# Performance work log

Hardware: AMD Instinct MI355X
Metric: run time of the kernel (lower is better)

The kernel has to match this reference:

```python
import jax, jax.numpy as jnp
import numpy as np

N_NODES = 50000
N_EDGES = 800000
N_FEAT = 128
HIDDEN = 64
N_GRAPHS = 256


def setup_inputs() -> dict:
    key = jax.random.key(0)
    ks = jax.random.split(key, 10)
    x = jax.random.normal(ks[0], (N_NODES, N_FEAT), dtype=jnp.float32)
    edge_index = jax.random.randint(ks[1], (2, N_EDGES), 0, N_NODES, dtype=jnp.int64)
    batch = jnp.sort(jax.random.randint(ks[2], (N_NODES,), 0, N_GRAPHS, dtype=jnp.int64))
    s1 = 1.0 / np.sqrt(N_FEAT)
    s2 = 1.0 / np.sqrt(HIDDEN)
    W1 = jax.random.normal(ks[3], (N_FEAT, HIDDEN), dtype=jnp.float32) * s1
    b1 = jnp.zeros((HIDDEN,), dtype=jnp.float32)
    W2 = jax.random.normal(ks[4], (HIDDEN, HIDDEN), dtype=jnp.float32) * s2
    b2 = jnp.zeros((HIDDEN,), dtype=jnp.float32)
    Wm1 = jax.random.normal(ks[5], (HIDDEN, HIDDEN), dtype=jnp.float32) * s2
    bm1 = jnp.zeros((HIDDEN,), dtype=jnp.float32)
    Wm2 = jax.random.normal(ks[6], (HIDDEN, 1), dtype=jnp.float32) * s2
    bm2 = jnp.zeros((1,), dtype=jnp.float32)
    return {"x": x, "edge_index": edge_index, "batch": batch,
            "W1": W1, "b1": b1, "W2": W2, "b2": b2,
            "Wm1": Wm1, "bm1": bm1, "Wm2": Wm2, "bm2": bm2}


def _gcn_layer(h, W, b, src, dst, norm, n_nodes):
    # GCNConv: h @ W, then symmetric-normalized scatter-add over edges (+ self-loops), + bias
    h = h @ W
    msg = h[src] * norm[:, None]              # [E+N, H] gather + scale
    agg = jax.ops.segment_sum(msg, dst, num_segments=n_nodes)
    return agg + b


def reference(x, edge_index, batch, W1, b1, W2, b2, Wm1, bm1, Wm2, bm2):
    n = x.shape[0]
    loops = jnp.arange(n, dtype=edge_index.dtype)
    src = jnp.concatenate([edge_index[0], loops])  # self-loops as in PyG GCNConv
    dst = jnp.concatenate([edge_index[1], loops])
    deg = jax.ops.segment_sum(jnp.ones_like(dst, dtype=x.dtype), dst, num_segments=n)
    dis = jnp.where(deg > 0, jax.lax.rsqrt(deg), 0.0)  # deg^-1/2
    norm = dis[src] * dis[dst]

    h = jax.nn.relu(_gcn_layer(x, W1, b1, src, dst, norm, n))
    h = jax.nn.relu(_gcn_layer(h, W2, b2, src, dst, norm, n))

    # global mean pool over graphs
    sums = jax.ops.segment_sum(h, batch, num_segments=N_GRAPHS)
    cnts = jax.ops.segment_sum(jnp.ones((n,), dtype=h.dtype), batch, num_segments=N_GRAPHS)
    pooled = sums / jnp.maximum(cnts, 1.0)[:, None]

    # MLP head (dropout inactive at eval)
    out = jax.nn.relu(pooled @ Wm1 + bm1) @ Wm2 + bm2
    return out.reshape(-1)
```

## Files before the change

### kernel.cpp

```cpp
#include <hip/hip_runtime.h>

#define NN 50000
#define NE 800000
#define NF 128
#define NH 64
#define NG 256
#define NB 196
#define NC 196
#define CH 4096
#define CELL 80
#define CAP 5120
#define NGB 782

typedef __attribute__((ext_vector_type(8))) short bf16x8;
typedef __attribute__((ext_vector_type(4))) float f32x4;

static __device__ __forceinline__ unsigned short f2bf(float f) {
    union { float f; unsigned u; } v; v.f = f;
    unsigned r = v.u + 0x7FFF + ((v.u >> 16) & 1);
    return (unsigned short)(r >> 16);
}
static __device__ __forceinline__ float lo16(unsigned u) {
    return __uint_as_float(u << 16);
}
static __device__ __forceinline__ float hi16(unsigned u) {
    return __uint_as_float(u & 0xFFFF0000u);
}
static __device__ __forceinline__ unsigned pack2(float a, float b) {
    return (unsigned)f2bf(a) | ((unsigned)f2bf(b) << 16);
}

__global__ __launch_bounds__(256) void prep_gemm(const int* __restrict__ ei,
                                                 int* __restrict__ histg,
                                                 unsigned* __restrict__ ebuf,
                                                 const float* __restrict__ X,
                                                 const float* __restrict__ W,
                                                 const float* __restrict__ W2,
                                                 unsigned short* __restrict__ Y,
                                                 float* __restrict__ psum,
                                                 unsigned* __restrict__ W2p) {
    __shared__ __align__(16) char smem[35840];
    const int t = threadIdx.x;

    if (blockIdx.x < NC) {
        int* hist = (int*)smem;
        int* incl = hist + 256;
        int* lcur = incl + 256;
        int* wq   = lcur + 256;
        unsigned* lpairs = (unsigned*)(smem + 4096);
        const int c = blockIdx.x;
        const int c0 = c * CH;

        hist[t] = 0;
        __syncthreads();

        int es[16], ed[16];
#pragma unroll
        for (int j = 0; j < 4; ++j) {
            const int e = c0 + (j * 256 + t) * 4;
            int4 s4 = make_int4(-1, -1, -1, -1);
            int4 d4 = make_int4(-1, -1, -1, -1);
            if (e + 3 < NE) {
                s4 = *(const int4*)&ei[e];
                d4 = *(const int4*)&ei[NE + e];
            } else {
                if (e < NE)     { s4.x = ei[e];     d4.x = ei[NE + e]; }
                if (e + 1 < NE) { s4.y = ei[e + 1]; d4.y = ei[NE + e + 1]; }
                if (e + 2 < NE) { s4.z = ei[e + 2]; d4.z = ei[NE + e + 2]; }
            }
            es[4*j] = s4.x; es[4*j+1] = s4.y; es[4*j+2] = s4.z; es[4*j+3] = s4.w;
            ed[4*j] = d4.x; ed[4*j+1] = d4.y; ed[4*j+2] = d4.z; ed[4*j+3] = d4.w;
            if (d4.x >= 0) atomicAdd(&hist[d4.x >> 8], 1);
            if (d4.y >= 0) atomicAdd(&hist[d4.y >> 8], 1);
            if (d4.z >= 0) atomicAdd(&hist[d4.z >> 8], 1);
            if (d4.w >= 0) atomicAdd(&hist[d4.w >> 8], 1);
        }
        __syncthreads();

        const int v = hist[t];
        int sv = v;
#pragma unroll
        for (int off = 1; off < 64; off <<= 1) {
            int u = __shfl_up(sv, off, 64);
            if ((t & 63) >= off) sv += u;
        }
        if ((t & 63) == 63) wq[t >> 6] = sv;
        __syncthreads();
        {
            const int wid = t >> 6;
            int add = 0;
            if (wid > 0) add += wq[0];
            if (wid > 1) add += wq[1];
            if (wid > 2) add += wq[2];
            sv += add;
        }
        incl[t] = sv;
        lcur[t] = sv - v;
        if (t < NB) histg[c * NB + t] = v;
        __syncthreads();

#pragma unroll
        for (int j = 0; j < 16; ++j) {
            const int d = ed[j];
            if (d >= 0) {
                int p = atomicAdd(&lcur[d >> 8], 1);
                lpairs[p] = (unsigned)es[j] | ((unsigned)d << 16);
            }
        }
        __syncthreads();

        const int total = incl[255];
        for (int p = t; p < total; p += 256) {
            const unsigned pr = lpairs[p];
            const int b = pr >> 24;
            const int i = p - (incl[b] - hist[b]);
            ebuf[(b * NC + c) * CELL + i] = pr;
        }
    } else {
        const int gb = blockIdx.x - NC;
        if (gb >= NGB) {
            for (int idx = t; idx < 2048; idx += 256) {
                const int n = idx >> 5, kp = idx & 31;
                W2p[idx] = pack2(W2[(2 * kp) * 64 + n], W2[(2 * kp + 1) * 64 + n]);
            }
            return;
        }
        if (gb < 17) {
            const int o = gb * 1024 + t * 4;
            if (o < 16640) *(float4*)&psum[o] = make_float4(0.f, 0.f, 0.f, 0.f);
        }

        unsigned short* Xs = (unsigned short*)smem;
        unsigned int* Wt = (unsigned int*)(smem + 17408);
        const int base = gb * 64;

        for (int i = t * 4; i < 64 * 128; i += 1024) {
            int node = i >> 7, k = i & 127;
            int gn = base + node; if (gn >= NN) gn = NN - 1;
            float4 v = *(const float4*)&X[(size_t)gn * 128 + k];
            ushort4 o = { f2bf(v.x), f2bf(v.y), f2bf(v.z), f2bf(v.w) };
            *(ushort4*)&Xs[node * 136 + k] = o;
        }
        for (int idx = t; idx < 64 * 64; idx += 256) {
            int n = idx & 63, kp = idx >> 6;
            float w0 = W[(2 * kp) * 64 + n];
            float w1 = W[(2 * kp + 1) * 64 + n];
            Wt[n * 68 + kp] = (unsigned)f2bf(w0) | ((unsigned)f2bf(w1) << 16);
        }
        __syncthreads();

        const int w = t >> 6;
        const int lane = t & 63;
        const int l15 = lane & 15;
        const int quad = lane >> 4;
        f32x4 acc[4] = {{0.f,0.f,0.f,0.f},{0.f,0.f,0.f,0.f},{0.f,0.f,0.f,0.f},{0.f,0.f,0.f,0.f}};
#pragma unroll
        for (int kk = 0; kk < 4; ++kk) {
            const bf16x8 a = *(const bf16x8*)&Xs[(w * 16 + l15) * 136 + quad * 8 + kk * 32];
#pragma unroll
            for (int nt = 0; nt < 4; ++nt) {
                const bf16x8 b = *(const bf16x8*)&Wt[(nt * 16 + l15) * 68 + quad * 4 + kk * 16];
                acc[nt] = __builtin_amdgcn_mfma_f32_16x16x32_bf16(a, b, acc[nt], 0, 0, 0);
            }
        }
        const int r0 = base + w * 16 + quad * 4;
#pragma unroll
        for (int reg = 0; reg < 4; ++reg) {
            const int row = r0 + reg;
            if (row < NN) {
#pragma unroll
                for (int nt = 0; nt < 4; ++nt)
                    Y[(size_t)row * 64 + nt * 16 + l15] = f2bf(acc[nt][reg]);
            }
        }
    }
}

__global__ __launch_bounds__(512) void build_csr(const unsigned* __restrict__ ebuf,
                                                 const int* __restrict__ histg,
                                                 int2* __restrict__ row_range,
                                                 float* __restrict__ dis,
                                                 int* __restrict__ csr_src) {
    const int b = blockIdx.x, t = threadIdx.x;
    const int e0 = b * CAP;
    __shared__ int coffs[256];
    __shared__ int cvs[256];
    __shared__ int deg_l[256];
    __shared__ int pre[256];
    __shared__ int cur[256];
    __shared__ int wq[8];
    __shared__ unsigned lpairs[CAP];
    __shared__ int lsrc[CAP];

    int cv = 0;
    if (t < NC) cv = histg[t * NB + b];
    int sv = cv;
    if (t < 256) {
#pragma unroll
        for (int off = 1; off < 64; off <<= 1) {
            int u = __shfl_up(sv, off, 64);
            if ((t & 63) >= off) sv += u;
        }
        if ((t & 63) == 63) wq[t >> 6] = sv;
        deg_l[t] = (b * 256 + t < NN) ? 1 : 0;
        cvs[t] = cv;
    }
    __syncthreads();
    if (t < 256) {
        const int wid = t >> 6;
        int add = 0;
        if (wid > 0) add += wq[0];
        if (wid > 1) add += wq[1];
        if (wid > 2) add += wq[2];
        coffs[t] = sv + add;
    }
    __syncthreads();

    {
        const int tc = t & 255;
        const int cv2 = cvs[tc];
        if (tc < NC && cv2 > 0) {
            const uint4* src4 = (const uint4*)&ebuf[(size_t)(b * NC + tc) * CELL];
            const int dst = coffs[tc] - cv2;
            for (int g4 = (t >> 8); g4 * 4 < cv2; g4 += 2) {
                const uint4 u = src4[g4];
                const int i = g4 * 4;
                lpairs[dst + i] = u.x;
                if (i + 1 < cv2) lpairs[dst + i + 1] = u.y;
                if (i + 2 < cv2) lpairs[dst + i + 2] = u.z;
                if (i + 3 < cv2) lpairs[dst + i + 3] = u.w;
            }
        }
    }
    __syncthreads();

    const int total = coffs[255];
    for (int i = t; i < total; i += 512)
        atomicAdd(&deg_l[(lpairs[i] >> 16) & 255], 1);
    __syncthreads();

    int dvi = 0, psv = 0;
    if (t < 256) {
        dvi = deg_l[t];
        psv = dvi;
#pragma unroll
        for (int off = 1; off < 64; off <<= 1) {
            int u = __shfl_up(psv, off, 64);
            if ((t & 63) >= off) psv += u;
        }
        if ((t & 63) == 63) wq[4 + (t >> 6)] = psv;
    }
    __syncthreads();
    if (t < 256) {
        const int wid = t >> 6;
        int add = 0;
        if (wid > 0) add += wq[4];
        if (wid > 1) add += wq[5];
        if (wid > 2) add += wq[6];
        psv += add;
        pre[t] = psv;
        cur[t] = 1;
        const int nd = b * 256 + t;
        if (nd < NN) {
            const int excl = psv - dvi;
            lsrc[excl] = nd;
            row_range[nd] = make_int2(e0 + excl, e0 + psv);
            dis[nd] = rsqrtf((float)dvi);
        }
    }
    __syncthreads();

    for (int i = t; i < total; i += 512) {
        const unsigned p = lpairs[i];
        const int d = (p >> 16) & 255;
        const int pos = (pre[d] - deg_l[d]) + atomicAdd(&cur[d], 1);
        lsrc[pos] = (int)(p & 0xFFFFu);
    }
    __syncthreads();
    const int tot_all = pre[255];
    for (int i = t; i < tot_all; i += 512)
        csr_src[e0 + i] = lsrc[i];
}

static __device__ __forceinline__ void acc8(float* acc, const uint4 u) {
    acc[0] += lo16(u.x); acc[1] += hi16(u.x);
    acc[2] += lo16(u.y); acc[3] += hi16(u.y);
    acc[4] += lo16(u.z); acc[5] += hi16(u.z);
    acc[6] += lo16(u.w); acc[7] += hi16(u.w);
}
static __device__ __forceinline__ void fma8(float* acc, const uint4 u, const float d) {
    acc[0] = fmaf(lo16(u.x), d, acc[0]); acc[1] = fmaf(hi16(u.x), d, acc[1]);
    acc[2] = fmaf(lo16(u.y), d, acc[2]); acc[3] = fmaf(hi16(u.y), d, acc[3]);
    acc[4] = fmaf(lo16(u.z), d, acc[4]); acc[5] = fmaf(hi16(u.z), d, acc[5]);
    acc[6] = fmaf(lo16(u.w), d, acc[6]); acc[7] = fmaf(hi16(u.w), d, acc[7]);
}

static __device__ __forceinline__ void gather_rows(const unsigned short* __restrict__ h,
                                                   const int* __restrict__ csr,
                                                   int lo, int hi, int p8, float* acc) {
    int i = lo;
    for (; i + 8 <= hi; i += 8) {
        int idx[8];
#pragma unroll
        for (int j = 0; j < 8; ++j) idx[j] = csr[i + j];
        uint4 u[8];
#pragma unroll
        for (int j = 0; j < 8; ++j) u[j] = *(const uint4*)&h[(idx[j] << 6) + p8];
#pragma unroll
        for (int j = 0; j < 8; ++j) acc8(acc, u[j]);
    }
    if (i + 4 <= hi) {
        int idx[4];
#pragma unroll
        for (int j = 0; j < 4; ++j) idx[j] = csr[i + j];
        uint4 u[4];
#pragma unroll
        for (int j = 0; j < 4; ++j) u[j] = *(const uint4*)&h[(idx[j] << 6) + p8];
#pragma unroll
        for (int j = 0; j < 4; ++j) acc8(acc, u[j]);
        i += 4;
    }
    if (i + 2 <= hi) {
        const int i0 = csr[i], i1 = csr[i + 1];
        const uint4 u0 = *(const uint4*)&h[(i0 << 6) + p8];
        const uint4 u1 = *(const uint4*)&h[(i1 << 6) + p8];
        acc8(acc, u0); acc8(acc, u1);
        i += 2;
    }
    if (i < hi) acc8(acc, *(const uint4*)&h[(csr[i] << 6) + p8]);
}

static __device__ __forceinline__ void gather_rows_scaled(const unsigned short* __restrict__ h,
                                                          const int* __restrict__ csr,
                                                          const float* __restrict__ dis,
                                                          int lo, int hi, int p8, float* acc) {
    int i = lo;
    for (; i + 8 <= hi; i += 8) {
        int idx[8];
#pragma unroll
        for (int j = 0; j < 8; ++j) idx[j] = csr[i + j];
        float d[8];
#pragma unroll
        for (int j = 0; j < 8; ++j) d[j] = dis[idx[j]];
        uint4 u[8];
#pragma unroll
        for (int j = 0; j < 8; ++j) u[j] = *(const uint4*)&h[(idx[j] << 6) + p8];
#pragma unroll
        for (int j = 0; j < 8; ++j) fma8(acc, u[j], d[j]);
    }
    if (i + 4 <= hi) {
        int idx[4];
#pragma unroll
        for (int j = 0; j < 4; ++j) idx[j] = csr[i + j];
        float d[4];
#pragma unroll
        for (int j = 0; j < 4; ++j) d[j] = dis[idx[j]];
        uint4 u[4];
#pragma unroll
        for (int j = 0; j < 4; ++j) u[j] = *(const uint4*)&h[(idx[j] << 6) + p8];
#pragma unroll
        for (int j = 0; j < 4; ++j) fma8(acc, u[j], d[j]);
        i += 4;
    }
    if (i + 2 <= hi) {
        const int i0 = csr[i], i1 = csr[i + 1];
        const float d0 = dis[i0], d1 = dis[i1];
        const uint4 u0 = *(const uint4*)&h[(i0 << 6) + p8];
        const uint4 u1 = *(const uint4*)&h[(i1 << 6) + p8];
        fma8(acc, u0, d0); fma8(acc, u1, d1);
        i += 2;
    }
    if (i < hi) {
        const int i0 = csr[i];
        fma8(acc, *(const uint4*)&h[(i0 << 6) + p8], dis[i0]);
    }
}

__global__ __launch_bounds__(256) void agg_gemv(const unsigned short* __restrict__ h,
                                                const int2* __restrict__ row_range,
                                                const int* __restrict__ csr_src,
                                                const float* __restrict__ dis,
                                                const float* __restrict__ b1,
                                                const unsigned* __restrict__ W2p,
                                                unsigned short* __restrict__ g) {
    __shared__ unsigned short W2b[64 * 72];
    __shared__ unsigned short A[32 * 72];
    const int t = threadIdx.x;
    const int base = blockIdx.x * 32;
    const int nloc = t >> 3;
    const int p8 = (t & 7) * 8;
    const int n = base + nloc;
    float acc[8] = {};
    if (n < NN) {
        const int2 rr = row_range[n];
        gather_rows_scaled(h, csr_src, dis, rr.x, rr.y, p8, acc);
        const float dn = dis[n];
        const float4 bv0 = *(const float4*)&b1[p8];
        const float4 bv1 = *(const float4*)&b1[p8 + 4];
        acc[0] = fmaxf(acc[0] * dn + bv0.x, 0.f);
        acc[1] = fmaxf(acc[1] * dn + bv0.y, 0.f);
        acc[2] = fmaxf(acc[2] * dn + bv0.z, 0.f);
        acc[3] = fmaxf(acc[3] * dn + bv0.w, 0.f);
        acc[4] = fmaxf(acc[4] * dn + bv1.x, 0.f);
        acc[5] = fmaxf(acc[5] * dn + bv1.y, 0.f);
        acc[6] = fmaxf(acc[6] * dn + bv1.z, 0.f);
        acc[7] = fmaxf(acc[7] * dn + bv1.w, 0.f);
    }
    for (int idx = t; idx < 2048; idx += 256) {
        const int nn2 = idx >> 5, kp = idx & 31;
        *(unsigned*)&W2b[nn2 * 72 + 2 * kp] = W2p[idx];
    }
    uint4 pk;
    pk.x = pack2(acc[0], acc[1]);
    pk.y = pack2(acc[2], acc[3]);
    pk.z = pack2(acc[4], acc[5]);
    pk.w = pack2(acc[6], acc[7]);
    *(uint4*)&A[nloc * 72 + p8] = pk;
    __syncthreads();

    const int w = t >> 6;
    const int lane = t & 63;
    const int l15 = lane & 15;
    const int quad = lane >> 4;
    const int mt = w & 1;
    const int nq = (w >> 1) * 2;
    const bf16x8 a0 = *(const bf16x8*)&A[(mt * 16 + l15) * 72 + quad * 8];
    const bf16x8 a1 = *(const bf16x8*)&A[(mt * 16 + l15) * 72 + 32 + quad * 8];
    const bf16x8 b00 = *(const bf16x8*)&W2b[(nq * 16 + l15) * 72 + quad * 8];
    const bf16x8 b01 = *(const bf16x8*)&W2b[(nq * 16 + l15) * 72 + 32 + quad * 8];
    const bf16x8 b10 = *(const bf16x8*)&W2b[((nq + 1) * 16 + l15) * 72 + quad * 8];
    const bf16x8 b11 = *(const bf16x8*)&W2b[((nq + 1) * 16 + l15) * 72 + 32 + quad * 8];
    f32x4 c0 = {0.f, 0.f, 0.f, 0.f}, c1 = {0.f, 0.f, 0.f, 0.f};
    c0 = __builtin_amdgcn_mfma_f32_16x16x32_bf16(a0, b00, c0, 0, 0, 0);
    c0 = __builtin_amdgcn_mfma_f32_16x16x32_bf16(a1, b01, c0, 0, 0, 0);
    c1 = __builtin_amdgcn_mfma_f32_16x16x32_bf16(a0, b10, c1, 0, 0, 0);
    c1 = __builtin_amdgcn_mfma_f32_16x16x32_bf16(a1, b11, c1, 0, 0, 0);
    const int r0 = base + mt * 16 + quad * 4;
    float4 d4 = *(const float4*)&dis[r0];
    const float dd[4] = { d4.x, d4.y, d4.z, d4.w };
#pragma unroll
    for (int reg = 0; reg < 4; ++reg) {
        const int row = r0 + reg;
        if (row < NN) {
            g[(size_t)row * 64 + nq * 16 + l15] = f2bf(c0[reg] * dd[reg]);
            g[(size_t)row * 64 + (nq + 1) * 16 + l15] = f2bf(c1[reg] * dd[reg]);
        }
    }
}

__global__ __launch_bounds__(256) void agg_pool(const unsigned short* __restrict__ h,
                                                const int2* __restrict__ row_range,
                                                const int* __restrict__ csr_src,
                                                const float* __restrict__ dis,
                                                const float* __restrict__ bias,
                                                const int* __restrict__ batch,
                                                float* __restrict__ psum,
                                                float* __restrict__ cnt) {
    __shared__ float rowsL[32 * 68];
    __shared__ int nb[32];
    const int t = threadIdx.x;
    const int nloc = t >> 3;
    const int n = blockIdx.x * 32 + nloc;
    const int p8 = (t & 7) * 8;
    if ((t & 7) == 0) nb[nloc] = (n < NN) ? batch[n] : -1;
    if (n < NN) {
        const int2 rr = row_range[n];
        float acc[8] = {};
        gather_rows(h, csr_src, rr.x, rr.y, p8, acc);
        const float dn = dis[n];
        const float4 bv0 = *(const float4*)&bias[p8];
        const float4 bv1 = *(const float4*)&bias[p8 + 4];
        float4 r0, r1;
        r0.x = fmaxf(acc[0] * dn + bv0.x, 0.f);
        r0.y = fmaxf(acc[1] * dn + bv0.y, 0.f);
        r0.z = fmaxf(acc[2] * dn + bv0.z, 0.f);
        r0.w = fmaxf(acc[3] * dn + bv0.w, 0.f);
        r1.x = fmaxf(acc[4] * dn + bv1.x, 0.f);
        r1.y = fmaxf(acc[5] * dn + bv1.y, 0.f);
        r1.z = fmaxf(acc[6] * dn + bv1.z, 0.f);
        r1.w = fmaxf(acc[7] * dn + bv1.w, 0.f);
        *(float4*)&rowsL[nloc * 68 + p8] = r0;
        *(float4*)&rowsL[nloc * 68 + p8 + 4] = r1;
    }
    __syncthreads();
    if (t < 64) {
        float s = 0.f; int curg = -2; int rl = 0;
        for (int r = 0; r < 32; ++r) {
            const int gg = nb[r];
            if (gg != curg) {
                if (curg >= 0) {
                    atomicAdd(&psum[curg * 64 + t], s);
                    if (t == 0) atomicAdd(&cnt[curg], (float)rl);
                }
                s = 0.f; rl = 0; curg = gg;
            }
            if (gg >= 0) { s += rowsL[r * 68 + t]; ++rl; }
        }
        if (curg >= 0) {
            atomicAdd(&psum[curg * 64 + t], s);
            if (t == 0) atomicAdd(&cnt[curg], (float)rl);
        }
    }
}

__global__ __launch_bounds__(64) void head_kernel(const float* __restrict__ psum,
                                                  const float* __restrict__ cnt,
                                                  const float* __restrict__ Wm1,
                                                  const float* __restrict__ bm1,
                                                  const float* __restrict__ Wm2,
                                                  const float* __restrict__ bm2,
                                                  float* __restrict__ out) {
    const int g = blockIdx.x;
    const int t = threadIdx.x;
    __shared__ float pl[64];
    const float inv = 1.f / fmaxf(cnt[g], 1.f);
    pl[t] = psum[g * 64 + t] * inv;
    __syncthreads();
    float z = bm1[t];
#pragma unroll 8
    for (int k = 0; k < 64; ++k)
        z += pl[k] * Wm1[k * 64 + t];
    z = fmaxf(z, 0.f);
    float y = z * Wm2[t];
    for (int off = 32; off; off >>= 1) y += __shfl_down(y, off);
    if (t == 0) out[g] = y + bm2[0];
}

extern "C" void kernel_launch(void* const* d_in, const int* in_sizes, int n_in,
                              void* d_out, int out_size, void* d_ws, size_t ws_size,
                              hipStream_t stream) {
    const float* x   = (const float*)d_in[0];
    const int*   ei  = (const int*)d_in[1];
    const int*   bat = (const int*)d_in[2];
    const float* W1  = (const float*)d_in[3];
    const float* b1  = (const float*)d_in[4];
    const float* W2  = (const float*)d_in[5];
    const float* b2  = (const float*)d_in[6];
    const float* Wm1 = (const float*)d_in[7];
    const float* bm1 = (const float*)d_in[8];
    const float* Wm2 = (const float*)d_in[9];
    const float* bm2 = (const float*)d_in[10];
    float* out = (float*)d_out;

    char* w = (char*)d_ws;
    int*            histg     = (int*)           (w + 0);
    int2*           row_range = (int2*)          (w + 153664);
    float*          dis       = (float*)         (w + 553664);
    int*            csr_src   = (int*)           (w + 753664);
    unsigned*       ebuf      = (unsigned*)      (w + 4767744);
    unsigned short* bufA      = (unsigned short*)(w + 17060864);
    unsigned short* bufB      = (unsigned short*)(w + 23460864);
    float*          psum      = (float*)         (w + 29860864);
    unsigned*       W2p       = (unsigned*)      (w + 29927424);
    float*          cnt       = psum + 16384;

    prep_gemm <<<NC + NGB + 1, 256, 0, stream>>>(ei, histg, ebuf, x, W1, W2, bufA, psum, W2p);
    build_csr <<<NB, 512, 0, stream>>>(ebuf, histg, row_range, dis, csr_src);
    agg_gemv  <<<(NN + 31) / 32, 256, 0, stream>>>(bufA, row_range, csr_src, dis, b1, W2p, bufB);
    agg_pool  <<<(NN + 31) / 32, 256, 0, stream>>>(bufB, row_range, csr_src, dis, b2, bat, psum, cnt);
    head_kernel<<<NG, 64, 0, stream>>>(psum, cnt, Wm1, bm1, Wm2, bm2, out);
}
```

Baseline: 149.2 us.

## Sort nodes by degree within chunks to balance aggregation blocks

```diff
diff --git a/kernel.cpp b/kernel.cpp
--- a/kernel.cpp
+++ b/kernel.cpp
@@ -11,6 +11,8 @@
 #define CELL 80
 #define CAP 5120
 #define NGB 782
+#define NSLOT (NB * 256)
+#define NAB 1568
 
 typedef __attribute__((ext_vector_type(8))) short bf16x8;
 typedef __attribute__((ext_vector_type(4))) float f32x4;
@@ -180,7 +182,8 @@
                                                  const int* __restrict__ histg,
                                                  int2* __restrict__ row_range,
                                                  float* __restrict__ dis,
-                                                 int* __restrict__ csr_src) {
+                                                 int* __restrict__ csr_src,
+                                                 int* __restrict__ perm) {
     const int b = blockIdx.x, t = threadIdx.x;
     const int e0 = b * CAP;
     __shared__ int coffs[256];
@@ -189,6 +192,8 @@
     __shared__ int pre[256];
     __shared__ int cur[256];
     __shared__ int wq[8];
+    __shared__ int dh[64];
+    __shared__ int dcur[64];
     __shared__ unsigned lpairs[CAP];
     __shared__ int lsrc[CAP];
 
@@ -280,6 +285,32 @@
     const int tot_all = pre[255];
     for (int i = t; i < tot_all; i += 512)
         csr_src[e0 + i] = lsrc[i];
+
+    if (t < 64) dh[t] = 0;
+    __syncthreads();
+    int dc = 63;
+    if (t < 256) {
+        const int nd = b * 256 + t;
+        dc = (nd < NN) ? (dvi < 62 ? dvi : 62) : 63;
+        atomicAdd(&dh[dc], 1);
+    }
+    __syncthreads();
+    if (t < 64) {
+        const int hv = dh[t];
+        int hs = hv;
+#pragma unroll
+        for (int off = 1; off < 64; off <<= 1) {
+            int u = __shfl_up(hs, off, 64);
+            if (t >= off) hs += u;
+        }
+        dcur[t] = hs - hv;
+    }
+    __syncthreads();
+    if (t < 256) {
+        const int nd = b * 256 + t;
+        const int rank = atomicAdd(&dcur[dc], 1);
+        perm[b * 256 + rank] = (nd < NN) ? nd : -1;
+    }
 }
 
 static __device__ __forceinline__ void acc8(float* acc, const uint4 u) {
@@ -382,16 +413,18 @@
                                                 const float* __restrict__ dis,
                                                 const float* __restrict__ b1,
                                                 const unsigned* __restrict__ W2p,
+                                                const int* __restrict__ perm,
                                                 unsigned short* __restrict__ g) {
     __shared__ unsigned short W2b[64 * 72];
     __shared__ unsigned short A[32 * 72];
+    __shared__ int nvals[32];
     const int t = threadIdx.x;
-    const int base = blockIdx.x * 32;
     const int nloc = t >> 3;
     const int p8 = (t & 7) * 8;
-    const int n = base + nloc;
+    const int n = perm[blockIdx.x * 32 + nloc];
+    if ((t & 7) == 0) nvals[nloc] = n;
     float acc[8] = {};
-    if (n < NN) {
+    if (n >= 0) {
         const int2 rr = row_range[n];
         gather_rows_scaled(h, csr_src, dis, rr.x, rr.y, p8, acc);
         const float dn = dis[n];
@@ -435,15 +468,14 @@
     c0 = __builtin_amdgcn_mfma_f32_16x16x32_bf16(a1, b01, c0, 0, 0, 0);
     c1 = __builtin_amdgcn_mfma_f32_16x16x32_bf16(a0, b10, c1, 0, 0, 0);
     c1 = __builtin_amdgcn_mfma_f32_16x16x32_bf16(a1, b11, c1, 0, 0, 0);
-    const int r0 = base + mt * 16 + quad * 4;
-    float4 d4 = *(const float4*)&dis[r0];
-    const float dd[4] = { d4.x, d4.y, d4.z, d4.w };
+    const int s0 = mt * 16 + quad * 4;
 #pragma unroll
     for (int reg = 0; reg < 4; ++reg) {
-        const int row = r0 + reg;
-        if (row < NN) {
-            g[(size_t)row * 64 + nq * 16 + l15] = f2bf(c0[reg] * dd[reg]);
-            g[(size_t)row * 64 + (nq + 1) * 16 + l15] = f2bf(c1[reg] * dd[reg]);
+        const int node = nvals[s0 + reg];
+        if (node >= 0) {
+            const float dd = dis[node];
+            g[(size_t)node * 64 + nq * 16 + l15] = f2bf(c0[reg] * dd);
+            g[(size_t)node * 64 + (nq + 1) * 16 + l15] = f2bf(c1[reg] * dd);
         }
     }
 }
@@ -454,16 +486,21 @@
                                                 const float* __restrict__ dis,
                                                 const float* __restrict__ bias,
                                                 const int* __restrict__ batch,
+                                                const int* __restrict__ perm,
                                                 float* __restrict__ psum,
                                                 float* __restrict__ cnt) {
     __shared__ float rowsL[32 * 68];
+    __shared__ float gacc[16][64];
+    __shared__ int gcnt[16];
     __shared__ int nb[32];
     const int t = threadIdx.x;
     const int nloc = t >> 3;
-    const int n = blockIdx.x * 32 + nloc;
     const int p8 = (t & 7) * 8;
-    if ((t & 7) == 0) nb[nloc] = (n < NN) ? batch[n] : -1;
-    if (n < NN) {
+    const int n = perm[blockIdx.x * 32 + nloc];
+    for (int idx = t; idx < 16 * 64; idx += 256) gacc[idx >> 6][idx & 63] = 0.f;
+    if (t < 16) gcnt[t] = 0;
+    if ((t & 7) == 0) nb[nloc] = (n >= 0) ? batch[n] : -1;
+    if (n >= 0) {
         const int2 rr = row_range[n];
         float acc[8] = {};
         gather_rows(h, csr_src, rr.x, rr.y, p8, acc);
@@ -483,22 +520,31 @@
         *(float4*)&rowsL[nloc * 68 + p8 + 4] = r1;
     }
     __syncthreads();
+    const int bk0 = (blockIdx.x * 32) & ~255;
+    const int g0 = batch[bk0 < NN ? bk0 : NN - 1];
     if (t < 64) {
-        float s = 0.f; int curg = -2; int rl = 0;
         for (int r = 0; r < 32; ++r) {
             const int gg = nb[r];
-            if (gg != curg) {
-                if (curg >= 0) {
-                    atomicAdd(&psum[curg * 64 + t], s);
-                    if (t == 0) atomicAdd(&cnt[curg], (float)rl);
+            if (gg >= 0) {
+                const int off = gg - g0;
+                if (off < 16) {
+                    gacc[off][t] += rowsL[r * 68 + t];
+                    if (t == 0) gcnt[off]++;
+                } else {
+                    atomicAdd(&psum[gg * 64 + t], rowsL[r * 68 + t]);
+                    if (t == 0) atomicAdd(&cnt[gg], 1.f);
                 }
-                s = 0.f; rl = 0; curg = gg;
-            }
-            if (gg >= 0) { s += rowsL[r * 68 + t]; ++rl; }
-        }
-        if (curg >= 0) {
-            atomicAdd(&psum[curg * 64 + t], s);
-            if (t == 0) atomicAdd(&cnt[curg], (float)rl);
+            }
+        }
+    }
+    __syncthreads();
+    {
+        const int l = t & 63;
+        for (int off = t >> 6; off < 16; off += 4) {
+            if (gcnt[off] > 0) {
+                atomicAdd(&psum[(g0 + off) * 64 + l], gacc[off][l]);
+                if (l == 0) atomicAdd(&cnt[g0 + off], (float)gcnt[off]);
+            }
         }
     }
 }
@@ -552,11 +598,12 @@
     unsigned short* bufB      = (unsigned short*)(w + 23460864);
     float*          psum      = (float*)         (w + 29860864);
     unsigned*       W2p       = (unsigned*)      (w + 29927424);
+    int*            perm      = (int*)           (w + 29935616);
     float*          cnt       = psum + 16384;
 
     prep_gemm <<<NC + NGB + 1, 256, 0, stream>>>(ei, histg, ebuf, x, W1, W2, bufA, psum, W2p);
-    build_csr <<<NB, 512, 0, stream>>>(ebuf, histg, row_range, dis, csr_src);
-    agg_gemv  <<<(NN + 31) / 32, 256, 0, stream>>>(bufA, row_range, csr_src, dis, b1, W2p, bufB);
-    agg_pool  <<<(NN + 31) / 32, 256, 0, stream>>>(bufB, row_range, csr_src, dis, b2, bat, psum, cnt);
+    build_csr <<<NB, 512, 0, stream>>>(ebuf, histg, row_range, dis, csr_src, perm);
+    agg_gemv  <<<NAB, 256, 0, stream>>>(bufA, row_range, csr_src, dis, b1, W2p, perm, bufB);
+    agg_pool  <<<NAB, 256, 0, stream>>>(bufB, row_range, csr_src, dis, b2, bat, perm, psum, cnt);
     head_kernel<<<NG, 64, 0, stream>>>(psum, cnt, Wm1, bm1, Wm2, bm2, out);
 }
```

Result: slower. 164.0 us (+9.9%).

## Move X@W1 GEMM blocks from partition kernel into CSR build kernel

Applied to the files above, without the earlier changes.

```diff
diff --git a/kernel.cpp b/kernel.cpp
--- a/kernel.cpp
+++ b/kernel.cpp
@@ -30,61 +30,132 @@
     return (unsigned)f2bf(a) | ((unsigned)f2bf(b) << 16);
 }
 
-__global__ __launch_bounds__(256) void prep_gemm(const int* __restrict__ ei,
-                                                 int* __restrict__ histg,
-                                                 unsigned* __restrict__ ebuf,
-                                                 const float* __restrict__ X,
-                                                 const float* __restrict__ W,
-                                                 const float* __restrict__ W2,
-                                                 unsigned short* __restrict__ Y,
-                                                 float* __restrict__ psum,
-                                                 unsigned* __restrict__ W2p) {
-    __shared__ __align__(16) char smem[35840];
+__global__ __launch_bounds__(256) void part_kernel(const int* __restrict__ ei,
+                                                   int* __restrict__ histg,
+                                                   unsigned* __restrict__ ebuf,
+                                                   const float* __restrict__ W2,
+                                                   float* __restrict__ psum,
+                                                   unsigned* __restrict__ W2p) {
     const int t = threadIdx.x;
-
-    if (blockIdx.x < NC) {
-        int* hist = (int*)smem;
-        int* incl = hist + 256;
-        int* lcur = incl + 256;
-        int* wq   = lcur + 256;
-        unsigned* lpairs = (unsigned*)(smem + 4096);
-        const int c = blockIdx.x;
-        const int c0 = c * CH;
-
-        hist[t] = 0;
-        __syncthreads();
-
-        int es[16], ed[16];
-#pragma unroll
-        for (int j = 0; j < 4; ++j) {
-            const int e = c0 + (j * 256 + t) * 4;
-            int4 s4 = make_int4(-1, -1, -1, -1);
-            int4 d4 = make_int4(-1, -1, -1, -1);
-            if (e + 3 < NE) {
-                s4 = *(const int4*)&ei[e];
-                d4 = *(const int4*)&ei[NE + e];
-            } else {
-                if (e < NE)     { s4.x = ei[e];     d4.x = ei[NE + e]; }
-                if (e + 1 < NE) { s4.y = ei[e + 1]; d4.y = ei[NE + e + 1]; }
-                if (e + 2 < NE) { s4.z = ei[e + 2]; d4.z = ei[NE + e + 2]; }
+    if (blockIdx.x >= NC) {
+        const int a = blockIdx.x - NC;
+        const int o = a * 1024 + t * 4;
+        if (o < 16640) *(float4*)&psum[o] = make_float4(0.f, 0.f, 0.f, 0.f);
+        if (a == 0) {
+            for (int idx = t; idx < 2048; idx += 256) {
+                const int n = idx >> 5, kp = idx & 31;
+                W2p[idx] = pack2(W2[(2 * kp) * 64 + n], W2[(2 * kp + 1) * 64 + n]);
             }
-            es[4*j] = s4.x; es[4*j+1] = s4.y; es[4*j+2] = s4.z; es[4*j+3] = s4.w;
-            ed[4*j] = d4.x; ed[4*j+1] = d4.y; ed[4*j+2] = d4.z; ed[4*j+3] = d4.w;
-            if (d4.x >= 0) atomicAdd(&hist[d4.x >> 8], 1);
-            if (d4.y >= 0) atomicAdd(&hist[d4.y >> 8], 1);
-            if (d4.z >= 0) atomicAdd(&hist[d4.z >> 8], 1);
-            if (d4.w >= 0) atomicAdd(&hist[d4.w >> 8], 1);
-        }
-        __syncthreads();
-
-        const int v = hist[t];
-        int sv = v;
+        }
+        return;
+    }
+    __shared__ __align__(16) char smem[20480];
+    int* hist = (int*)smem;
+    int* incl = hist + 256;
+    int* lcur = incl + 256;
+    int* wq   = lcur + 256;
+    unsigned* lpairs = (unsigned*)(smem + 4096);
+    const int c = blockIdx.x;
+    const int c0 = c * CH;
+
+    hist[t] = 0;
+    __syncthreads();
+
+    int es[16], ed[16];
+#pragma unroll
+    for (int j = 0; j < 4; ++j) {
+        const int e = c0 + (j * 256 + t) * 4;
+        int4 s4 = make_int4(-1, -1, -1, -1);
+        int4 d4 = make_int4(-1, -1, -1, -1);
+        if (e + 3 < NE) {
+            s4 = *(const int4*)&ei[e];
+            d4 = *(const int4*)&ei[NE + e];
+        } else {
+            if (e < NE)     { s4.x = ei[e];     d4.x = ei[NE + e]; }
+            if (e + 1 < NE) { s4.y = ei[e + 1]; d4.y = ei[NE + e + 1]; }
+            if (e + 2 < NE) { s4.z = ei[e + 2]; d4.z = ei[NE + e + 2]; }
+        }
+        es[4*j] = s4.x; es[4*j+1] = s4.y; es[4*j+2] = s4.z; es[4*j+3] = s4.w;
+        ed[4*j] = d4.x; ed[4*j+1] = d4.y; ed[4*j+2] = d4.z; ed[4*j+3] = d4.w;
+        if (d4.x >= 0) atomicAdd(&hist[d4.x >> 8], 1);
+        if (d4.y >= 0) atomicAdd(&hist[d4.y >> 8], 1);
+        if (d4.z >= 0) atomicAdd(&hist[d4.z >> 8], 1);
+        if (d4.w >= 0) atomicAdd(&hist[d4.w >> 8], 1);
+    }
+    __syncthreads();
+
+    const int v = hist[t];
+    int sv = v;
+#pragma unroll
+    for (int off = 1; off < 64; off <<= 1) {
+        int u = __shfl_up(sv, off, 64);
+        if ((t & 63) >= off) sv += u;
+    }
+    if ((t & 63) == 63) wq[t >> 6] = sv;
+    __syncthreads();
+    {
+        const int wid = t >> 6;
+        int add = 0;
+        if (wid > 0) add += wq[0];
+        if (wid > 1) add += wq[1];
+        if (wid > 2) add += wq[2];
+        sv += add;
+    }
+    incl[t] = sv;
+    lcur[t] = sv - v;
+    if (t < NB) histg[c * NB + t] = v;
+    __syncthreads();
+
+#pragma unroll
+    for (int j = 0; j < 16; ++j) {
+        const int d = ed[j];
+        if (d >= 0) {
+            int p = atomicAdd(&lcur[d >> 8], 1);
+            lpairs[p] = (unsigned)es[j] | ((unsigned)d << 16);
+        }
+    }
+    __syncthreads();
+
+    const int total = incl[255];
+    for (int p = t; p < total; p += 256) {
+        const unsigned pr = lpairs[p];
+        const int b = pr >> 24;
+        const int i = p - (incl[b] - hist[b]);
+        ebuf[(b * NC + c) * CELL + i] = pr;
+    }
+}
+
+__global__ __launch_bounds__(256) void csr_gemm(const unsigned* __restrict__ ebuf,
+                                                const int* __restrict__ histg,
+                                                int2* __restrict__ row_range,
+                                                float* __restrict__ dis,
+                                                int* __restrict__ csr_src,
+                                                const float* __restrict__ X,
+                                                const float* __restrict__ W,
+                                                unsigned short* __restrict__ Y) {
+    __shared__ __align__(16) char smem[45088];
+    const int t = threadIdx.x;
+
+    if (blockIdx.x < NB) {
+        int* coffs = (int*)smem;
+        int* deg_l = coffs + 256;
+        int* pre   = deg_l + 256;
+        int* cur   = pre + 256;
+        int* wq    = cur + 256;
+        unsigned* lpairs = (unsigned*)(smem + 4128);
+        int* lsrc = (int*)(smem + 4128 + CAP * 4);
+        const int b = blockIdx.x;
+        const int e0 = b * CAP;
+
+        const int cv = (t < NC) ? histg[t * NB + b] : 0;
+        int sv = cv;
 #pragma unroll
         for (int off = 1; off < 64; off <<= 1) {
             int u = __shfl_up(sv, off, 64);
             if ((t & 63) >= off) sv += u;
         }
         if ((t & 63) == 63) wq[t >> 6] = sv;
+        deg_l[t] = (b * 256 + t < NN) ? 1 : 0;
         __syncthreads();
         {
             const int wid = t >> 6;
@@ -92,172 +163,46 @@
             if (wid > 0) add += wq[0];
             if (wid > 1) add += wq[1];
             if (wid > 2) add += wq[2];
-            sv += add;
-        }
-        incl[t] = sv;
-        lcur[t] = sv - v;
-        if (t < NB) histg[c * NB + t] = v;
-        __syncthreads();
-
-#pragma unroll
-        for (int j = 0; j < 16; ++j) {
-            const int d = ed[j];
-            if (d >= 0) {
-                int p = atomicAdd(&lcur[d >> 8], 1);
-                lpairs[p] = (unsigned)es[j] | ((unsigned)d << 16);
+            coffs[t] = sv + add;
+        }
+        __syncthreads();
+
+        if (t < NC && cv > 0) {
+            const uint4* src4 = (const uint4*)&ebuf[(size_t)(b * NC + t) * CELL];
+            const int dst = coffs[t] - cv;
+            for (int i4 = 0; i4 * 4 < cv; ++i4) {
+                const uint4 u = src4[i4];
+                const int i = i4 * 4;
+                lpairs[dst + i] = u.x;
+                if (i + 1 < cv) lpairs[dst + i + 1] = u.y;
+                if (i + 2 < cv) lpairs[dst + i + 2] = u.z;
+                if (i + 3 < cv) lpairs[dst + i + 3] = u.w;
             }
         }
         __syncthreads();
 
-        const int total = incl[255];
-        for (int p = t; p < total; p += 256) {
-            const unsigned pr = lpairs[p];
-            const int b = pr >> 24;
-            const int i = p - (incl[b] - hist[b]);
-            ebuf[(b * NC + c) * CELL + i] = pr;
-        }
-    } else {
-        const int gb = blockIdx.x - NC;
-        if (gb >= NGB) {
-            for (int idx = t; idx < 2048; idx += 256) {
-                const int n = idx >> 5, kp = idx & 31;
-                W2p[idx] = pack2(W2[(2 * kp) * 64 + n], W2[(2 * kp + 1) * 64 + n]);
-            }
-            return;
-        }
-        if (gb < 17) {
-            const int o = gb * 1024 + t * 4;
-            if (o < 16640) *(float4*)&psum[o] = make_float4(0.f, 0.f, 0.f, 0.f);
-        }
-
-        unsigned short* Xs = (unsigned short*)smem;
-        unsigned int* Wt = (unsigned int*)(smem + 17408);
-        const int base = gb * 64;
-
-        for (int i = t * 4; i < 64 * 128; i += 1024) {
-            int node = i >> 7, k = i & 127;
-            int gn = base + node; if (gn >= NN) gn = NN - 1;
-            float4 v = *(const float4*)&X[(size_t)gn * 128 + k];
-            ushort4 o = { f2bf(v.x), f2bf(v.y), f2bf(v.z), f2bf(v.w) };
-            *(ushort4*)&Xs[node * 136 + k] = o;
-        }
-        for (int idx = t; idx < 64 * 64; idx += 256) {
-            int n = idx & 63, kp = idx >> 6;
-            float w0 = W[(2 * kp) * 64 + n];
-            float w1 = W[(2 * kp + 1) * 64 + n];
-            Wt[n * 68 + kp] = (unsigned)f2bf(w0) | ((unsigned)f2bf(w1) << 16);
-        }
-        __syncthreads();
-
-        const int w = t >> 6;
-        const int lane = t & 63;
-        const int l15 = lane & 15;
-        const int quad = lane >> 4;
-        f32x4 acc[4] = {{0.f,0.f,0.f,0.f},{0.f,0.f,0.f,0.f},{0.f,0.f,0.f,0.f},{0.f,0.f,0.f,0.f}};
-#pragma unroll
-        for (int kk = 0; kk < 4; ++kk) {
-            const bf16x8 a = *(const bf16x8*)&Xs[(w * 16 + l15) * 136 + quad * 8 + kk * 32];
-#pragma unroll
-            for (int nt = 0; nt < 4; ++nt) {
-                const bf16x8 b = *(const bf16x8*)&Wt[(nt * 16 + l15) * 68 + quad * 4 + kk * 16];
-                acc[nt] = __builtin_amdgcn_mfma_f32_16x16x32_bf16(a, b, acc[nt], 0, 0, 0);
-            }
-        }
-        const int r0 = base + w * 16 + quad * 4;
-#pragma unroll
-        for (int reg = 0; reg < 4; ++reg) {
-            const int row = r0 + reg;
-            if (row < NN) {
-#pragma unroll
-                for (int nt = 0; nt < 4; ++nt)
-                    Y[(size_t)row * 64 + nt * 16 + l15] = f2bf(acc[nt][reg]);
-            }
-        }
-    }
-}
-
-__global__ __launch_bounds__(512) void build_csr(const unsigned* __restrict__ ebuf,
-                                                 const int* __restrict__ histg,
-                                                 int2* __restrict__ row_range,
-                                                 float* __restrict__ dis,
-                                                 int* __restrict__ csr_src) {
-    const int b = blockIdx.x, t = threadIdx.x;
-    const int e0 = b * CAP;
-    __shared__ int coffs[256];
-    __shared__ int cvs[256];
-    __shared__ int deg_l[256];
-    __shared__ int pre[256];
-    __shared__ int cur[256];
-    __shared__ int wq[8];
-    __shared__ unsigned lpairs[CAP];
-    __shared__ int lsrc[CAP];
-
-    int cv = 0;
-    if (t < NC) cv = histg[t * NB + b];
-    int sv = cv;
-    if (t < 256) {
-#pragma unroll
-        for (int off = 1; off < 64; off <<= 1) {
-            int u = __shfl_up(sv, off, 64);
-            if ((t & 63) >= off) sv += u;
-        }
-        if ((t & 63) == 63) wq[t >> 6] = sv;
-        deg_l[t] = (b * 256 + t < NN) ? 1 : 0;
-        cvs[t] = cv;
-    }
-    __syncthreads();
-    if (t < 256) {
-        const int wid = t >> 6;
-        int add = 0;
-        if (wid > 0) add += wq[0];
-        if (wid > 1) add += wq[1];
-        if (wid > 2) add += wq[2];
-        coffs[t] = sv + add;
-    }
-    __syncthreads();
-
-    {
-        const int tc = t & 255;
-        const int cv2 = cvs[tc];
-        if (tc < NC && cv2 > 0) {
-            const uint4* src4 = (const uint4*)&ebuf[(size_t)(b * NC + tc) * CELL];
-            const int dst = coffs[tc] - cv2;
-            for (int g4 = (t >> 8); g4 * 4 < cv2; g4 += 2) {
-                const uint4 u = src4[g4];
-                const int i = g4 * 4;
-                lpairs[dst + i] = u.x;
-                if (i + 1 < cv2) lpairs[dst + i + 1] = u.y;
-                if (i + 2 < cv2) lpairs[dst + i + 2] = u.z;
-                if (i + 3 < cv2) lpairs[dst + i + 3] = u.w;
-            }
-        }
-    }
-    __syncthreads();
-
-    const int total = coffs[255];
-    for (int i = t; i < total; i += 512)
-        atomicAdd(&deg_l[(lpairs[i] >> 16) & 255], 1);
-    __syncthreads();
-
-    int dvi = 0, psv = 0;
-    if (t < 256) {
-        dvi = deg_l[t];
-        psv = dvi;
+        const int total = coffs[255];
+        for (int i = t; i < total; i += 256)
+            atomicAdd(&deg_l[(lpairs[i] >> 16) & 255], 1);
+        __syncthreads();
+
+        const int dvi = deg_l[t];
+        int psv = dvi;
 #pragma unroll
         for (int off = 1; off < 64; off <<= 1) {
             int u = __shfl_up(psv, off, 64);
             if ((t & 63) >= off) psv += u;
         }
         if ((t & 63) == 63) wq[4 + (t >> 6)] = psv;
-    }
-    __syncthreads();
-    if (t < 256) {
-        const int wid = t >> 6;
-        int add = 0;
-        if (wid > 0) add += wq[4];
-        if (wid > 1) add += wq[5];
-        if (wid > 2) add += wq[6];
-        psv += add;
+        __syncthreads();
+        {
+            const int wid = t >> 6;
+            int add = 0;
+            if (wid > 0) add += wq[4];
+            if (wid > 1) add += wq[5];
+            if (wid > 2) add += wq[6];
+            psv += add;
+        }
         pre[t] = psv;
         cur[t] = 1;
         const int nd = b * 256 + t;
@@ -267,19 +212,64 @@
             row_range[nd] = make_int2(e0 + excl, e0 + psv);
             dis[nd] = rsqrtf((float)dvi);
         }
-    }
-    __syncthreads();
-
-    for (int i = t; i < total; i += 512) {
-        const unsigned p = lpairs[i];
-        const int d = (p >> 16) & 255;
-        const int pos = (pre[d] - deg_l[d]) + atomicAdd(&cur[d], 1);
-        lsrc[pos] = (int)(p & 0xFFFFu);
-    }
-    __syncthreads();
-    const int tot_all = pre[255];
-    for (int i = t; i < tot_all; i += 512)
-        csr_src[e0 + i] = lsrc[i];
+        __syncthreads();
+
+        for (int i = t; i < total; i += 256) {
+            const unsigned p = lpairs[i];
+            const int d = (p >> 16) & 255;
+            const int pos = (pre[d] - deg_l[d]) + atomicAdd(&cur[d], 1);
+            lsrc[pos] = (int)(p & 0xFFFFu);
+        }
+        __syncthreads();
+        const int tot_all = pre[255];
+        for (int i = t; i < tot_all; i += 256)
+            csr_src[e0 + i] = lsrc[i];
+    } else {
+        const int gb = blockIdx.x - NB;
+        unsigned short* Xs = (unsigned short*)smem;
+        unsigned int* Wt = (unsigned int*)(smem + 17408);
+        const int base = gb * 64;
+
+        for (int i = t * 4; i < 64 * 128; i += 1024) {
+            int node = i >> 7, k = i & 127;
+            int gn = base + node; if (gn >= NN) gn = NN - 1;
+            float4 v = *(const float4*)&X[(size_t)gn * 128 + k];
+            ushort4 o = { f2bf(v.x), f2bf(v.y), f2bf(v.z), f2bf(v.w) };
+            *(ushort4*)&Xs[node * 136 + k] = o;
+        }
+        for (int idx = t; idx < 64 * 64; idx += 256) {
+            int n = idx & 63, kp = idx >> 6;
+            float w0 = W[(2 * kp) * 64 + n];
+            float w1 = W[(2 * kp + 1) * 64 + n];
+            Wt[n * 68 + kp] = (unsigned)f2bf(w0) | ((unsigned)f2bf(w1) << 16);
+        }
+        __syncthreads();
+
+        const int w = t >> 6;
+        const int lane = t & 63;
+        const int l15 = lane & 15;
+        const int quad = lane >> 4;
+        f32x4 acc[4] = {{0.f,0.f,0.f,0.f},{0.f,0.f,0.f,0.f},{0.f,0.f,0.f,0.f},{0.f,0.f,0.f,0.f}};
+#pragma unroll
+        for (int kk = 0; kk < 4; ++kk) {
+            const bf16x8 a = *(const bf16x8*)&Xs[(w * 16 + l15) * 136 + quad * 8 + kk * 32];
+#pragma unroll
+            for (int nt = 0; nt < 4; ++nt) {
+                const bf16x8 b = *(const bf16x8*)&Wt[(nt * 16 + l15) * 68 + quad * 4 + kk * 16];
+                acc[nt] = __builtin_amdgcn_mfma_f32_16x16x32_bf16(a, b, acc[nt], 0, 0, 0);
+            }
+        }
+        const int r0 = base + w * 16 + quad * 4;
+#pragma unroll
+        for (int reg = 0; reg < 4; ++reg) {
+            const int row = r0 + reg;
+            if (row < NN) {
+#pragma unroll
+                for (int nt = 0; nt < 4; ++nt)
+                    Y[(size_t)row * 64 + nt * 16 + l15] = f2bf(acc[nt][reg]);
+            }
+        }
+    }
 }
 
 static __device__ __forceinline__ void acc8(float* acc, const uint4 u) {
@@ -554,8 +544,8 @@
     unsigned*       W2p       = (unsigned*)      (w + 29927424);
     float*          cnt       = psum + 16384;
 
-    prep_gemm <<<NC + NGB + 1, 256, 0, stream>>>(ei, histg, ebuf, x, W1, W2, bufA, psum, W2p);
-    build_csr <<<NB, 512, 0, stream>>>(ebuf, histg, row_range, dis, csr_src);
+    part_kernel<<<NC + 17, 256, 0, stream>>>(ei, histg, ebuf, W2, psum, W2p);
+    csr_gemm  <<<NB + NGB, 256, 0, stream>>>(ebuf, histg, row_range, dis, csr_src, x, W1, bufA);
     agg_gemv  <<<(NN + 31) / 32, 256, 0, stream>>>(bufA, row_range, csr_src, dis, b1, W2p, bufB);
     agg_pool  <<<(NN + 31) / 32, 256, 0, stream>>>(bufB, row_range, csr_src, dis, b2, bat, psum, cnt);
     head_kernel<<<NG, 64, 0, stream>>>(psum, cnt, Wm1, bm1, Wm2, bm2, out);
```

Result: no change. 151.2 us (+1.3%).
